# Optimization experiments

Hardware: AMD Instinct MI355X
Metric: run time of the kernel (lower is better)

## Reference

```python
import jax, jax.numpy as jnp
import numpy as np

# Dimensions
N = 100000      # nodes
E = 500000      # edges
D_IN = 128      # in_channels
H, C = 2, 64    # heads, out_channels per head (out_channels=128)
T = 128         # time_enc.out_channels
MSG = 128       # msg_dim
EDGE_DIM = MSG + T  # 256
SCALE = 1.0 / np.sqrt(C)


def setup_inputs() -> dict:
    key = jax.random.key(0)
    ks = jax.random.split(key, 16)
    s = 0.05
    x = jax.random.normal(ks[0], (N, D_IN), dtype=jnp.float32)
    last_update = jax.random.uniform(ks[1], (N,), dtype=jnp.float32)
    edge_index = jax.random.randint(ks[2], (2, E), 0, N, dtype=jnp.int64)
    t = jax.random.uniform(ks[3], (E,), dtype=jnp.float32) + 1.0  # event times >= last_update typically
    msg = jax.random.normal(ks[4], (E, MSG), dtype=jnp.float32)
    # TimeEncoder: cos(Linear(1, T))
    time_w = jax.random.normal(ks[5], (T, 1), dtype=jnp.float32) * s
    time_b = jax.random.normal(ks[6], (T,), dtype=jnp.float32) * s
    # TransformerConv linear layers (PyG defaults: q/k/v with bias, edge without, skip with bias)
    Wq = jax.random.normal(ks[7], (D_IN, H * C), dtype=jnp.float32) * s
    bq = jnp.zeros((H * C,), dtype=jnp.float32)
    Wk = jax.random.normal(ks[8], (D_IN, H * C), dtype=jnp.float32) * s
    bk = jnp.zeros((H * C,), dtype=jnp.float32)
    Wv = jax.random.normal(ks[9], (D_IN, H * C), dtype=jnp.float32) * s
    bv = jnp.zeros((H * C,), dtype=jnp.float32)
    We = jax.random.normal(ks[10], (EDGE_DIM, H * C), dtype=jnp.float32) * s
    Wskip = jax.random.normal(ks[11], (D_IN, H * C), dtype=jnp.float32) * s
    bskip = jnp.zeros((H * C,), dtype=jnp.float32)
    return dict(x=x, last_update=last_update, edge_index=edge_index, t=t, msg=msg,
                time_w=time_w, time_b=time_b, Wq=Wq, bq=bq, Wk=Wk, bk=bk,
                Wv=Wv, bv=bv, We=We, Wskip=Wskip, bskip=bskip)


def reference(x, last_update, edge_index, t, msg, time_w, time_b,
              Wq, bq, Wk, bk, Wv, bv, We, Wskip, bskip):
    src, dst = edge_index[0], edge_index[1]
    # relative time encoding: cos(Linear(1, T)(rel_t))
    rel_t = t - last_update[src]                                   # [E]
    rel_t_enc = jnp.cos(rel_t[:, None] * time_w[:, 0][None, :] + time_b)  # [E, T]
    edge_attr = jnp.concatenate([rel_t_enc, msg], axis=-1)         # [E, EDGE_DIM]

    # TransformerConv (heads=H, per-head dim C, eval mode so no dropout)
    q = (x @ Wq + bq).reshape(N, H, C)
    k = (x @ Wk + bk).reshape(N, H, C)
    v = (x @ Wv + bv).reshape(N, H, C)
    e = (edge_attr @ We).reshape(E, H, C)

    k_j = k[src] + e                                               # [E, H, C]
    logits = jnp.sum(q[dst] * k_j, axis=-1) * SCALE                # [E, H]

    # segment softmax over destination nodes
    m = jax.ops.segment_max(logits, dst, num_segments=N)           # [N, H]
    p = jnp.exp(logits - m[dst])
    denom = jax.ops.segment_sum(p, dst, num_segments=N)
    alpha = p / (denom[dst] + 1e-16)                               # [E, H]

    msgs = (v[src] + e) * alpha[..., None]                         # [E, H, C]
    out = jax.ops.segment_sum(msgs, dst, num_segments=N).reshape(N, H * C)
    # root/skip connection
    return out + x @ Wskip + bskip
```

## Files before the change

### kernel.cpp

```cpp
#include <hip/hip_runtime.h>
#include <math.h>


#define SCALE_ATTN 0.125f
#define SCAN_CHUNK 512

typedef __attribute__((ext_vector_type(8))) short bf16x8;
typedef __attribute__((ext_vector_type(4))) float f32x4;

union AFrag { bf16x8 v; unsigned short u[8]; };

__device__ __forceinline__ unsigned short f2bf(float f) {
    unsigned int u = __float_as_uint(f);
    u += 0x7fffu + ((u >> 16) & 1u);
    return (unsigned short)(u >> 16);
}
__device__ __forceinline__ float bf2f(unsigned int lo16) {
    return __uint_as_float(lo16 << 16);
}
__device__ __forceinline__ void unpack8(uint4 u, float* f) {
    f[0] = bf2f(u.x & 0xffffu); f[1] = bf2f(u.x >> 16);
    f[2] = bf2f(u.y & 0xffffu); f[3] = bf2f(u.y >> 16);
    f[4] = bf2f(u.z & 0xffffu); f[5] = bf2f(u.z >> 16);
    f[6] = bf2f(u.w & 0xffffu); f[7] = bf2f(u.w >> 16);
}
__device__ __forceinline__ bf16x8 pack2(float4 a, float4 b) {
    AFrag f;
    f.u[0] = f2bf(a.x); f.u[1] = f2bf(a.y); f.u[2] = f2bf(a.z); f.u[3] = f2bf(a.w);
    f.u[4] = f2bf(b.x); f.u[5] = f2bf(b.y); f.u[6] = f2bf(b.z); f.u[7] = f2bf(b.w);
    return f.v;
}

__global__ __launch_bounds__(256) void k_zero(int4* __restrict__ p, int n4)
{
    const int i = blockIdx.x * 256 + threadIdx.x;
    if (i < n4) p[i] = make_int4(0, 0, 0, 0);
}

__global__ __launch_bounds__(512, 4) void k_node_mfma(
    const float4* __restrict__ x4,
    const float* __restrict__ Wq, const float* __restrict__ Wk,
    const float* __restrict__ Wv, const float* __restrict__ Ws,
    const float* __restrict__ bq, const float* __restrict__ bk,
    const float* __restrict__ bv, const float* __restrict__ bs,
    unsigned short* __restrict__ qb, unsigned short* __restrict__ kb,
    unsigned short* __restrict__ vb, float* __restrict__ outp,
    int N, int numTiles)
{
    __shared__ __align__(16) unsigned short sX[32 * 128];
    const int tid = threadIdx.x;
    const int w = tid >> 6, l = tid & 63;
    const int l15 = l & 15, lg = l >> 4;
    const int mat = w >> 1;
    const int colbase = (w & 1) * 64;

    const float* Wm = (mat == 0) ? Wq : (mat == 1) ? Wk : (mat == 2) ? Wv : Ws;
    const float* bm = (mat == 0) ? bq : (mat == 1) ? bk : (mat == 2) ? bv : bs;

    bf16x8 Bf[4][4];
    float bias[4];
    #pragma unroll
    for (int nt = 0; nt < 4; ++nt) {
        const int col = colbase + nt * 16 + l15;
        bias[nt] = bm[col];
        #pragma unroll
        for (int ks = 0; ks < 4; ++ks) {
            AFrag f;
            #pragma unroll
            for (int j = 0; j < 8; ++j)
                f.u[j] = f2bf(Wm[(ks * 32 + lg * 8 + j) * 128 + col]);
            Bf[ks][nt] = f.v;
        }
    }

    for (int tile = blockIdx.x; tile < numTiles; tile += gridDim.x) {
        {
            const int e = tid >> 4, k8 = tid & 15;
            const int row = min(tile * 32 + e, N - 1);
            const float4 a0 = x4[(size_t)row * 32 + k8 * 2];
            const float4 a1 = x4[(size_t)row * 32 + k8 * 2 + 1];
            const int byteoff = (e * 256 + k8 * 16) ^ ((e & 7) << 4);
            *(bf16x8*)((char*)sX + byteoff) = pack2(a0, a1);
        }
        __syncthreads();

        f32x4 acc[2][4];
        #pragma unroll
        for (int m = 0; m < 2; ++m)
            #pragma unroll
            for (int nt = 0; nt < 4; ++nt) acc[m][nt] = (f32x4)(0.f);

        #pragma unroll
        for (int m = 0; m < 2; ++m) {
            const int lrow = m * 16 + l15;
            #pragma unroll
            for (int ks = 0; ks < 4; ++ks) {
                const int byteoff = (lrow * 256 + ks * 64 + lg * 16) ^ ((lrow & 7) << 4);
                const bf16x8 a = *(const bf16x8*)((const char*)sX + byteoff);
                #pragma unroll
                for (int nt = 0; nt < 4; ++nt)
                    acc[m][nt] = __builtin_amdgcn_mfma_f32_16x16x32_bf16(a, Bf[ks][nt], acc[m][nt], 0, 0, 0);
            }
        }

        #pragma unroll
        for (int m = 0; m < 2; ++m) {
            #pragma unroll
            for (int nt = 0; nt < 4; ++nt) {
                const int col = colbase + nt * 16 + l15;
                #pragma unroll
                for (int r = 0; r < 4; ++r) {
                    const int node = tile * 32 + m * 16 + lg * 4 + r;
                    if (node < N) {
                        const float val = acc[m][nt][r] + bias[nt];
                        if (mat == 0)      qb[(size_t)node * 128 + col] = f2bf(val);
                        else if (mat == 1) kb[(size_t)node * 128 + col] = f2bf(val);
                        else if (mat == 2) vb[(size_t)node * 128 + col] = f2bf(val);
                        else               outp[(size_t)node * 128 + col] = val;
                    }
                }
            }
        }
        __syncthreads();
    }
}

__global__ __launch_bounds__(512, 4) void k_edge_mfma(
    const float4* __restrict__ msg4,
    const float* __restrict__ relo,
    const float4* __restrict__ tw4, const float4* __restrict__ tb4,
    const float* __restrict__ We,
    unsigned short* __restrict__ ebuf, int E, int numTiles)
{
    __shared__ __align__(16) unsigned short sWe[128 * 256];
    __shared__ __align__(16) unsigned short sMsg[64 * 128];
    const int tid = threadIdx.x;
    const int w = tid >> 6, l = tid & 63;
    const int l15 = l & 15, lg = l >> 4;
    const int msub = w >> 1;
    const int colbase = (w & 1) * 64;

    for (int c = tid; c < 4096; c += 512) {
        const int n = c >> 5, k0 = (c & 31) << 3;
        AFrag af;
        #pragma unroll
        for (int j = 0; j < 8; ++j) af.u[j] = f2bf(We[(k0 + j) * 128 + n]);
        const int byteoff = ((n << 9) + (k0 << 1)) ^ ((n & 7) << 4);
        *(bf16x8*)((char*)sWe + byteoff) = af.v;
    }
    __syncthreads();

    const int nrow = colbase + l15;
    const int swzW = (nrow & 7) << 4;

    for (int tile = blockIdx.x; tile < numTiles; tile += gridDim.x) {
        const int ebase = tile * 64;

        #pragma unroll
        for (int i = 0; i < 2; ++i) {
            const int U = tid * 2 + i;
            const int e = U >> 4, u = U & 15;
            const int er = min(ebase + e, E - 1);
            const float4 a0 = msg4[(size_t)er * 32 + u * 2];
            const float4 a1 = msg4[(size_t)er * 32 + u * 2 + 1];
            const int byteoff = (e << 8) + ((u ^ (e & 7)) << 4);
            *(bf16x8*)((char*)sMsg + byteoff) = pack2(a0, a1);
        }
        __syncthreads();

        const int erow = ebase + msub * 16 + l15;
        const float rel = relo[min(erow, E - 1)];

        f32x4 acc[4];
        #pragma unroll
        for (int i = 0; i < 4; ++i) acc[i] = (f32x4)(0.f);

        #pragma unroll
        for (int kk = 0; kk < 4; ++kk) {
            const int kbase = (kk << 5) + (lg << 3);

            const float4 tww = tw4[kbase >> 2];
            const float4 tw2 = tw4[(kbase >> 2) + 1];
            const float4 tbb = tb4[kbase >> 2];
            const float4 tb2 = tb4[(kbase >> 2) + 1];
            AFrag a;
            a.u[0] = f2bf(__cosf(fmaf(rel, tww.x, tbb.x)));
            a.u[1] = f2bf(__cosf(fmaf(rel, tww.y, tbb.y)));
            a.u[2] = f2bf(__cosf(fmaf(rel, tww.z, tbb.z)));
            a.u[3] = f2bf(__cosf(fmaf(rel, tww.w, tbb.w)));
            a.u[4] = f2bf(__cosf(fmaf(rel, tw2.x, tb2.x)));
            a.u[5] = f2bf(__cosf(fmaf(rel, tw2.y, tb2.y)));
            a.u[6] = f2bf(__cosf(fmaf(rel, tw2.z, tb2.z)));
            a.u[7] = f2bf(__cosf(fmaf(rel, tw2.w, tb2.w)));
            const int bC = ((nrow << 9) + (kbase << 1)) ^ swzW;
            #pragma unroll
            for (int nt = 0; nt < 4; ++nt) {
                const bf16x8 b = *(const bf16x8*)((const char*)sWe + (bC + (nt << 13)));
                acc[nt] = __builtin_amdgcn_mfma_f32_16x16x32_bf16(a.v, b, acc[nt], 0, 0, 0);
            }

            const int me = msub * 16 + l15;
            const int mu = (kk << 2) + lg;
            const int mbyte = (me << 8) + ((mu ^ (me & 7)) << 4);
            const bf16x8 am = *(const bf16x8*)((const char*)sMsg + mbyte);
            const int bM = ((nrow << 9) + ((128 + kbase) << 1)) ^ swzW;
            #pragma unroll
            for (int nt = 0; nt < 4; ++nt) {
                const bf16x8 b = *(const bf16x8*)((const char*)sWe + (bM + (nt << 13)));
                acc[nt] = __builtin_amdgcn_mfma_f32_16x16x32_bf16(am, b, acc[nt], 0, 0, 0);
            }
        }

        #pragma unroll
        for (int nt = 0; nt < 4; ++nt) {
            const int col = colbase + nt * 16 + l15;
            #pragma unroll
            for (int r = 0; r < 4; ++r) {
                const int er = ebase + msub * 16 + (lg << 2) + r;
                if (er < E) ebuf[(size_t)er * 128 + col] = f2bf(acc[nt][r]);
            }
        }
        __syncthreads();
    }
}

__global__ __launch_bounds__(256) void k_hist(
    const int* __restrict__ ei, int* __restrict__ counts, int E)
{
    int i = blockIdx.x * 256 + threadIdx.x;
    if (i < E) atomicAdd(&counts[ei[E + i]], 1);
}

__global__ __launch_bounds__(256) void k_scan_partial(
    const int* __restrict__ counts, int* __restrict__ partial, int N)
{
    const int base = blockIdx.x * SCAN_CHUNK;
    int v = 0;
    for (int i = threadIdx.x; i < SCAN_CHUNK; i += 256) {
        const int idx = base + i;
        if (idx < N) v += counts[idx];
    }
    __shared__ int red[4];
    #pragma unroll
    for (int off = 1; off < 64; off <<= 1) v += __shfl_xor(v, off);
    if ((threadIdx.x & 63) == 0) red[threadIdx.x >> 6] = v;
    __syncthreads();
    if (threadIdx.x == 0) partial[blockIdx.x] = red[0] + red[1] + red[2] + red[3];
}

__global__ __launch_bounds__(256) void k_scan_base(
    const int* __restrict__ partial, int* __restrict__ base, int nb)
{
    __shared__ int tmp[256];
    const int v = (threadIdx.x < nb) ? partial[threadIdx.x] : 0;
    tmp[threadIdx.x] = v;
    __syncthreads();
    for (int off = 1; off < 256; off <<= 1) {
        const int add = (threadIdx.x >= off) ? tmp[threadIdx.x - off] : 0;
        __syncthreads();
        tmp[threadIdx.x] += add;
        __syncthreads();
    }
    if (threadIdx.x < nb) base[threadIdx.x] = tmp[threadIdx.x] - v;
}

__global__ __launch_bounds__(256) void k_scan_final(
    const int* __restrict__ counts, const int* __restrict__ base,
    int* __restrict__ rowptr, int* __restrict__ cursor, int N)
{
    const int i0 = blockIdx.x * SCAN_CHUNK;
    __shared__ int tmp[256];
    const int ia = i0 + threadIdx.x * 2, ib = ia + 1;
    const int v0 = (ia < N) ? counts[ia] : 0;
    const int v1 = (ib < N) ? counts[ib] : 0;
    const int s = v0 + v1;
    tmp[threadIdx.x] = s;
    __syncthreads();
    for (int off = 1; off < 256; off <<= 1) {
        const int add = (threadIdx.x >= off) ? tmp[threadIdx.x - off] : 0;
        __syncthreads();
        tmp[threadIdx.x] += add;
        __syncthreads();
    }
    const int excl = tmp[threadIdx.x] - s + base[blockIdx.x];
    if (ia < N) { rowptr[ia] = excl;      cursor[ia] = excl; }
    if (ib < N) { rowptr[ib] = excl + v0; cursor[ib] = excl + v0; }
}

__global__ __launch_bounds__(256) void k_fill(
    const int* __restrict__ ei, const float* __restrict__ t,
    const float* __restrict__ lu, int* __restrict__ cursor,
    int* __restrict__ perm, int* __restrict__ srcp,
    float* __restrict__ relo, int E)
{
    int i = blockIdx.x * 256 + threadIdx.x;
    if (i < E) {
        const int s = ei[i];
        const int d = ei[E + i];
        const int pos = atomicAdd(&cursor[d], 1);
        perm[pos] = i;
        srcp[pos] = s;
        relo[i] = t[i] - lu[s];
    }
}

__global__ __launch_bounds__(256) void k_agg(
    const int* __restrict__ srcp, const int* __restrict__ perm,
    const int* __restrict__ rowptr, const int* __restrict__ counts,
    const uint4* __restrict__ qb4, const uint4* __restrict__ kb4,
    const uint4* __restrict__ vb4, const uint4* __restrict__ eb4,
    float4* __restrict__ out4, int N)
{
    const int d = blockIdx.x * 4 + (threadIdx.x >> 6);
    if (d >= N) return;
    const int l = threadIdx.x & 63;
    const int s16 = l & 15;
    const int eg = l >> 4;
    const int start = rowptr[d];
    const int deg = counts[d];

    float qf[8];
    unpack8(qb4[(size_t)d * 16 + s16], qf);
    float accf[8] = {0.f, 0.f, 0.f, 0.f, 0.f, 0.f, 0.f, 0.f};
    float denom = 0.f;

    for (int cbase = 0; cbase < deg; cbase += 64) {
        const int clen = min(deg - cbase, 64);
        int mySrc = 0, myEid = 0;
        if (l < clen) {
            mySrc = srcp[start + cbase + l];
            myEid = perm[start + cbase + l];
        }

        #pragma unroll 2
        for (int i = 0; i < clen; i += 4) {
            const int off = i + eg;
            const bool valid = off < clen;
            const int offc = valid ? off : 0;
            const int src = __shfl(mySrc, offc);
            const int eid = __shfl(myEid, offc);
            float kf[8], ef[8], vf[8];
            unpack8(kb4[(size_t)src * 16 + s16], kf);
            unpack8(eb4[(size_t)eid * 16 + s16], ef);
            unpack8(vb4[(size_t)src * 16 + s16], vf);
            float s = 0.f;
            #pragma unroll
            for (int j = 0; j < 8; ++j) s = fmaf(qf[j], kf[j] + ef[j], s);
            s += __shfl_xor(s, 1);
            s += __shfl_xor(s, 2);
            s += __shfl_xor(s, 4);
            const float p = valid ? __expf(s * SCALE_ATTN) : 0.f;
            denom += p;
            #pragma unroll
            for (int j = 0; j < 8; ++j) accf[j] = fmaf(p, vf[j] + ef[j], accf[j]);
        }
    }
    #pragma unroll
    for (int j = 0; j < 8; ++j) {
        accf[j] += __shfl_xor(accf[j], 16);
        accf[j] += __shfl_xor(accf[j], 32);
    }
    denom += __shfl_xor(denom, 16);
    denom += __shfl_xor(denom, 32);

    if (l < 16) {
        const float inv = 1.f / (denom + 1e-16f);
        float4* o = out4 + (size_t)d * 32 + s16 * 2;
        const float4 c0 = o[0];
        const float4 c1 = o[1];
        o[0] = make_float4(fmaf(accf[0], inv, c0.x), fmaf(accf[1], inv, c0.y),
                           fmaf(accf[2], inv, c0.z), fmaf(accf[3], inv, c0.w));
        o[1] = make_float4(fmaf(accf[4], inv, c1.x), fmaf(accf[5], inv, c1.y),
                           fmaf(accf[6], inv, c1.z), fmaf(accf[7], inv, c1.w));
    }
}

extern "C" void kernel_launch(void* const* d_in, const int* in_sizes, int n_in,
                              void* d_out, int out_size, void* d_ws, size_t ws_size,
                              hipStream_t stream)
{
    const float* x   = (const float*)d_in[0];
    const float* lu  = (const float*)d_in[1];
    const int*   ei  = (const int*)d_in[2];
    const float* t   = (const float*)d_in[3];
    const float* msg = (const float*)d_in[4];
    const float* tw  = (const float*)d_in[5];
    const float* tb  = (const float*)d_in[6];
    const float* Wq  = (const float*)d_in[7];
    const float* bq  = (const float*)d_in[8];
    const float* Wk  = (const float*)d_in[9];
    const float* bk  = (const float*)d_in[10];
    const float* Wv  = (const float*)d_in[11];
    const float* bv  = (const float*)d_in[12];
    const float* We  = (const float*)d_in[13];
    const float* Wsk = (const float*)d_in[14];
    const float* bsk = (const float*)d_in[15];

    const int N = in_sizes[1];
    const int E = in_sizes[3];
    float* out = (float*)d_out;

    char* ws = (char*)d_ws;
    unsigned short* qb = (unsigned short*)ws;  ws += (size_t)N * 128 * sizeof(unsigned short);
    unsigned short* kb = (unsigned short*)ws;  ws += (size_t)N * 128 * sizeof(unsigned short);
    unsigned short* vb = (unsigned short*)ws;  ws += (size_t)N * 128 * sizeof(unsigned short);
    unsigned short* eb = (unsigned short*)ws;  ws += (size_t)E * 128 * sizeof(unsigned short);
    int*   counts  = (int*)ws;   ws += (size_t)N * sizeof(int);
    int*   rowptr  = (int*)ws;   ws += (size_t)N * sizeof(int);
    int*   cursor  = (int*)ws;   ws += (size_t)N * sizeof(int);
    int*   perm    = (int*)ws;   ws += (size_t)E * sizeof(int);
    int*   srcp    = (int*)ws;   ws += (size_t)E * sizeof(int);
    float* relo    = (float*)ws; ws += (size_t)E * sizeof(float);
    int*   partial = (int*)ws;   ws += 512 * sizeof(int);
    int*   baseArr = (int*)ws;   ws += 512 * sizeof(int);

    const int nScan = (N + SCAN_CHUNK - 1) / SCAN_CHUNK;

    const int n4 = (N + 3) / 4;
    k_zero<<<(n4 + 255) / 256, 256, 0, stream>>>((int4*)counts, n4);

    k_hist<<<(E + 255) / 256, 256, 0, stream>>>(ei, counts, E);
    k_scan_partial<<<nScan, 256, 0, stream>>>(counts, partial, N);
    k_scan_base<<<1, 256, 0, stream>>>(partial, baseArr, nScan);
    k_scan_final<<<nScan, 256, 0, stream>>>(counts, baseArr, rowptr, cursor, N);
    k_fill<<<(E + 255) / 256, 256, 0, stream>>>(ei, t, lu, cursor, perm, srcp, relo, E);

    const int nTN = (N + 31) / 32;
    k_node_mfma<<<min(nTN, 1024), 512, 0, stream>>>(
        (const float4*)x, Wq, Wk, Wv, Wsk, bq, bk, bv, bsk,
        qb, kb, vb, out, N, nTN);

    const int nTE = (E + 63) / 64;
    k_edge_mfma<<<min(nTE, 512), 512, 0, stream>>>(
        (const float4*)msg, relo,
        (const float4*)tw, (const float4*)tb, We, eb, E, nTE);

    k_agg<<<(N + 3) / 4, 256, 0, stream>>>(
        srcp, perm, rowptr, counts,
        (const uint4*)qb, (const uint4*)kb, (const uint4*)vb, (const uint4*)eb,
        (float4*)out, N);
}
```

Before: 368.1 us.

## Store skip projection as bf16, restructure edge GEMM waves, skip invalid edge loads

The node kernel now writes the skip projection to a bf16 workspace buffer instead of fp32 into the output, and the aggregation kernel reads that buffer rather than re-reading the fp32 output. The edge GEMM drops to 256 threads per block, with each wave handling two 16-row edge tiles so every LDS weight fragment feeds two MFMAs, halving weight LDS reads. The aggregation loop skips the gather loads for invalid lanes. The skip connection loses precision through bf16 rounding, and the edge kernel has fewer waves per block, which reduces latency hiding.

```diff
diff --git a/kernel.cpp b/kernel.cpp
--- a/kernel.cpp
+++ b/kernel.cpp
@@ -44,7 +44,7 @@
     const float* __restrict__ bq, const float* __restrict__ bk,
     const float* __restrict__ bv, const float* __restrict__ bs,
     unsigned short* __restrict__ qb, unsigned short* __restrict__ kb,
-    unsigned short* __restrict__ vb, float* __restrict__ outp,
+    unsigned short* __restrict__ vb, unsigned short* __restrict__ skb,
     int N, int numTiles)
 {
     __shared__ __align__(16) unsigned short sX[32 * 128];
@@ -56,6 +56,7 @@
 
     const float* Wm = (mat == 0) ? Wq : (mat == 1) ? Wk : (mat == 2) ? Wv : Ws;
     const float* bm = (mat == 0) ? bq : (mat == 1) ? bk : (mat == 2) ? bv : bs;
+    unsigned short* dst = (mat == 0) ? qb : (mat == 1) ? kb : (mat == 2) ? vb : skb;
 
     bf16x8 Bf[4][4];
     float bias[4];
@@ -111,13 +112,8 @@
                 #pragma unroll
                 for (int r = 0; r < 4; ++r) {
                     const int node = tile * 32 + m * 16 + lg * 4 + r;
-                    if (node < N) {
-                        const float val = acc[m][nt][r] + bias[nt];
-                        if (mat == 0)      qb[(size_t)node * 128 + col] = f2bf(val);
-                        else if (mat == 1) kb[(size_t)node * 128 + col] = f2bf(val);
-                        else if (mat == 2) vb[(size_t)node * 128 + col] = f2bf(val);
-                        else               outp[(size_t)node * 128 + col] = val;
-                    }
+                    if (node < N)
+                        dst[(size_t)node * 128 + col] = f2bf(acc[m][nt][r] + bias[nt]);
                 }
             }
         }
@@ -125,7 +121,7 @@
     }
 }
 
-__global__ __launch_bounds__(512, 4) void k_edge_mfma(
+__global__ __launch_bounds__(256, 2) void k_edge_mfma(
     const float4* __restrict__ msg4,
     const float* __restrict__ relo,
     const float4* __restrict__ tw4, const float4* __restrict__ tb4,
@@ -137,10 +133,10 @@
     const int tid = threadIdx.x;
     const int w = tid >> 6, l = tid & 63;
     const int l15 = l & 15, lg = l >> 4;
-    const int msub = w >> 1;
-    const int colbase = (w & 1) * 64;
-
-    for (int c = tid; c < 4096; c += 512) {
+    const int ch = w & 1;
+    const int mp = w >> 1;
+
+    for (int c = tid; c < 4096; c += 256) {
         const int n = c >> 5, k0 = (c & 31) << 3;
         AFrag af;
         #pragma unroll
@@ -150,15 +146,12 @@
     }
     __syncthreads();
 
-    const int nrow = colbase + l15;
-    const int swzW = (nrow & 7) << 4;
-
     for (int tile = blockIdx.x; tile < numTiles; tile += gridDim.x) {
         const int ebase = tile * 64;
 
         #pragma unroll
-        for (int i = 0; i < 2; ++i) {
-            const int U = tid * 2 + i;
+        for (int i = 0; i < 4; ++i) {
+            const int U = tid + i * 256;
             const int e = U >> 4, u = U & 15;
             const int er = min(ebase + e, E - 1);
             const float4 a0 = msg4[(size_t)er * 32 + u * 2];
@@ -168,12 +161,14 @@
         }
         __syncthreads();
 
-        const int erow = ebase + msub * 16 + l15;
-        const float rel = relo[min(erow, E - 1)];
-
-        f32x4 acc[4];
-        #pragma unroll
-        for (int i = 0; i < 4; ++i) acc[i] = (f32x4)(0.f);
+        const int r0 = mp * 32 + l15;
+        const int r1 = r0 + 16;
+        const float rel0 = relo[min(ebase + r0, E - 1)];
+        const float rel1 = relo[min(ebase + r1, E - 1)];
+
+        f32x4 acc0[4], acc1[4];
+        #pragma unroll
+        for (int i = 0; i < 4; ++i) { acc0[i] = (f32x4)(0.f); acc1[i] = (f32x4)(0.f); }
 
         #pragma unroll
         for (int kk = 0; kk < 4; ++kk) {
@@ -183,41 +178,54 @@
             const float4 tw2 = tw4[(kbase >> 2) + 1];
             const float4 tbb = tb4[kbase >> 2];
             const float4 tb2 = tb4[(kbase >> 2) + 1];
-            AFrag a;
-            a.u[0] = f2bf(__cosf(fmaf(rel, tww.x, tbb.x)));
-            a.u[1] = f2bf(__cosf(fmaf(rel, tww.y, tbb.y)));
-            a.u[2] = f2bf(__cosf(fmaf(rel, tww.z, tbb.z)));
-            a.u[3] = f2bf(__cosf(fmaf(rel, tww.w, tbb.w)));
-            a.u[4] = f2bf(__cosf(fmaf(rel, tw2.x, tb2.x)));
-            a.u[5] = f2bf(__cosf(fmaf(rel, tw2.y, tb2.y)));
-            a.u[6] = f2bf(__cosf(fmaf(rel, tw2.z, tb2.z)));
-            a.u[7] = f2bf(__cosf(fmaf(rel, tw2.w, tb2.w)));
-            const int bC = ((nrow << 9) + (kbase << 1)) ^ swzW;
+            AFrag a0, a1;
+            a0.u[0] = f2bf(__cosf(fmaf(rel0, tww.x, tbb.x)));
+            a0.u[1] = f2bf(__cosf(fmaf(rel0, tww.y, tbb.y)));
+            a0.u[2] = f2bf(__cosf(fmaf(rel0, tww.z, tbb.z)));
+            a0.u[3] = f2bf(__cosf(fmaf(rel0, tww.w, tbb.w)));
+            a0.u[4] = f2bf(__cosf(fmaf(rel0, tw2.x, tb2.x)));
+            a0.u[5] = f2bf(__cosf(fmaf(rel0, tw2.y, tb2.y)));
+            a0.u[6] = f2bf(__cosf(fmaf(rel0, tw2.z, tb2.z)));
+            a0.u[7] = f2bf(__cosf(fmaf(rel0, tw2.w, tb2.w)));
+            a1.u[0] = f2bf(__cosf(fmaf(rel1, tww.x, tbb.x)));
+            a1.u[1] = f2bf(__cosf(fmaf(rel1, tww.y, tbb.y)));
+            a1.u[2] = f2bf(__cosf(fmaf(rel1, tww.z, tbb.z)));
+            a1.u[3] = f2bf(__cosf(fmaf(rel1, tww.w, tbb.w)));
+            a1.u[4] = f2bf(__cosf(fmaf(rel1, tw2.x, tb2.x)));
+            a1.u[5] = f2bf(__cosf(fmaf(rel1, tw2.y, tb2.y)));
+            a1.u[6] = f2bf(__cosf(fmaf(rel1, tw2.z, tb2.z)));
+            a1.u[7] = f2bf(__cosf(fmaf(rel1, tw2.w, tb2.w)));
+
+            const int mu = (kk << 2) + lg;
+            const bf16x8 am0 = *(const bf16x8*)((const char*)sMsg +
+                                 ((r0 << 8) + ((mu ^ (r0 & 7)) << 4)));
+            const bf16x8 am1 = *(const bf16x8*)((const char*)sMsg +
+                                 ((r1 << 8) + ((mu ^ (r1 & 7)) << 4)));
+
             #pragma unroll
             for (int nt = 0; nt < 4; ++nt) {
-                const bf16x8 b = *(const bf16x8*)((const char*)sWe + (bC + (nt << 13)));
-                acc[nt] = __builtin_amdgcn_mfma_f32_16x16x32_bf16(a.v, b, acc[nt], 0, 0, 0);
+                const int nrow = ch * 64 + nt * 16 + l15;
+                const int swz = (nrow & 7) << 4;
+                const bf16x8 bC = *(const bf16x8*)((const char*)sWe +
+                                   (((nrow << 9) + (kbase << 1)) ^ swz));
+                acc0[nt] = __builtin_amdgcn_mfma_f32_16x16x32_bf16(a0.v, bC, acc0[nt], 0, 0, 0);
+                acc1[nt] = __builtin_amdgcn_mfma_f32_16x16x32_bf16(a1.v, bC, acc1[nt], 0, 0, 0);
+                const bf16x8 bM = *(const bf16x8*)((const char*)sWe +
+                                   (((nrow << 9) + ((128 + kbase) << 1)) ^ swz));
+                acc0[nt] = __builtin_amdgcn_mfma_f32_16x16x32_bf16(am0, bM, acc0[nt], 0, 0, 0);
+                acc1[nt] = __builtin_amdgcn_mfma_f32_16x16x32_bf16(am1, bM, acc1[nt], 0, 0, 0);
             }
-
-            const int me = msub * 16 + l15;
-            const int mu = (kk << 2) + lg;
-            const int mbyte = (me << 8) + ((mu ^ (me & 7)) << 4);
-            const bf16x8 am = *(const bf16x8*)((const char*)sMsg + mbyte);
-            const int bM = ((nrow << 9) + ((128 + kbase) << 1)) ^ swzW;
-            #pragma unroll
-            for (int nt = 0; nt < 4; ++nt) {
-                const bf16x8 b = *(const bf16x8*)((const char*)sWe + (bM + (nt << 13)));
-                acc[nt] = __builtin_amdgcn_mfma_f32_16x16x32_bf16(am, b, acc[nt], 0, 0, 0);
-            }
         }
 
         #pragma unroll
         for (int nt = 0; nt < 4; ++nt) {
-            const int col = colbase + nt * 16 + l15;
+            const int col = ch * 64 + nt * 16 + l15;
             #pragma unroll
             for (int r = 0; r < 4; ++r) {
-                const int er = ebase + msub * 16 + (lg << 2) + r;
-                if (er < E) ebuf[(size_t)er * 128 + col] = f2bf(acc[nt][r]);
+                const int e0 = ebase + mp * 32 + (lg << 2) + r;
+                const int e1 = e0 + 16;
+                if (e0 < E) ebuf[(size_t)e0 * 128 + col] = f2bf(acc0[nt][r]);
+                if (e1 < E) ebuf[(size_t)e1 * 128 + col] = f2bf(acc1[nt][r]);
             }
         }
         __syncthreads();
@@ -309,7 +317,7 @@
     const int* __restrict__ rowptr, const int* __restrict__ counts,
     const uint4* __restrict__ qb4, const uint4* __restrict__ kb4,
     const uint4* __restrict__ vb4, const uint4* __restrict__ eb4,
-    float4* __restrict__ out4, int N)
+    const uint4* __restrict__ skb4, float4* __restrict__ out4, int N)
 {
     const int d = blockIdx.x * 4 + (threadIdx.x >> 6);
     if (d >= N) return;
@@ -339,20 +347,22 @@
             const int offc = valid ? off : 0;
             const int src = __shfl(mySrc, offc);
             const int eid = __shfl(myEid, offc);
-            float kf[8], ef[8], vf[8];
-            unpack8(kb4[(size_t)src * 16 + s16], kf);
-            unpack8(eb4[(size_t)eid * 16 + s16], ef);
-            unpack8(vb4[(size_t)src * 16 + s16], vf);
-            float s = 0.f;
-            #pragma unroll
-            for (int j = 0; j < 8; ++j) s = fmaf(qf[j], kf[j] + ef[j], s);
-            s += __shfl_xor(s, 1);
-            s += __shfl_xor(s, 2);
-            s += __shfl_xor(s, 4);
-            const float p = valid ? __expf(s * SCALE_ATTN) : 0.f;
-            denom += p;
-            #pragma unroll
-            for (int j = 0; j < 8; ++j) accf[j] = fmaf(p, vf[j] + ef[j], accf[j]);
+            if (valid) {
+                float kf[8], ef[8], vf[8];
+                unpack8(kb4[(size_t)src * 16 + s16], kf);
+                unpack8(eb4[(size_t)eid * 16 + s16], ef);
+                unpack8(vb4[(size_t)src * 16 + s16], vf);
+                float s = 0.f;
+                #pragma unroll
+                for (int j = 0; j < 8; ++j) s = fmaf(qf[j], kf[j] + ef[j], s);
+                s += __shfl_xor(s, 1);
+                s += __shfl_xor(s, 2);
+                s += __shfl_xor(s, 4);
+                const float p = __expf(s * SCALE_ATTN);
+                denom += p;
+                #pragma unroll
+                for (int j = 0; j < 8; ++j) accf[j] = fmaf(p, vf[j] + ef[j], accf[j]);
+            }
         }
     }
     #pragma unroll
@@ -365,13 +375,13 @@
 
     if (l < 16) {
         const float inv = 1.f / (denom + 1e-16f);
+        float sk[8];
+        unpack8(skb4[(size_t)d * 16 + s16], sk);
         float4* o = out4 + (size_t)d * 32 + s16 * 2;
-        const float4 c0 = o[0];
-        const float4 c1 = o[1];
-        o[0] = make_float4(fmaf(accf[0], inv, c0.x), fmaf(accf[1], inv, c0.y),
-                           fmaf(accf[2], inv, c0.z), fmaf(accf[3], inv, c0.w));
-        o[1] = make_float4(fmaf(accf[4], inv, c1.x), fmaf(accf[5], inv, c1.y),
-                           fmaf(accf[6], inv, c1.z), fmaf(accf[7], inv, c1.w));
+        o[0] = make_float4(fmaf(accf[0], inv, sk[0]), fmaf(accf[1], inv, sk[1]),
+                           fmaf(accf[2], inv, sk[2]), fmaf(accf[3], inv, sk[3]));
+        o[1] = make_float4(fmaf(accf[4], inv, sk[4]), fmaf(accf[5], inv, sk[5]),
+                           fmaf(accf[6], inv, sk[6]), fmaf(accf[7], inv, sk[7]));
     }
 }
 
@@ -401,10 +411,11 @@
     float* out = (float*)d_out;
 
     char* ws = (char*)d_ws;
-    unsigned short* qb = (unsigned short*)ws;  ws += (size_t)N * 128 * sizeof(unsigned short);
-    unsigned short* kb = (unsigned short*)ws;  ws += (size_t)N * 128 * sizeof(unsigned short);
-    unsigned short* vb = (unsigned short*)ws;  ws += (size_t)N * 128 * sizeof(unsigned short);
-    unsigned short* eb = (unsigned short*)ws;  ws += (size_t)E * 128 * sizeof(unsigned short);
+    unsigned short* qb  = (unsigned short*)ws;  ws += (size_t)N * 128 * sizeof(unsigned short);
+    unsigned short* kb  = (unsigned short*)ws;  ws += (size_t)N * 128 * sizeof(unsigned short);
+    unsigned short* vb  = (unsigned short*)ws;  ws += (size_t)N * 128 * sizeof(unsigned short);
+    unsigned short* skb = (unsigned short*)ws;  ws += (size_t)N * 128 * sizeof(unsigned short);
+    unsigned short* eb  = (unsigned short*)ws;  ws += (size_t)E * 128 * sizeof(unsigned short);
     int*   counts  = (int*)ws;   ws += (size_t)N * sizeof(int);
     int*   rowptr  = (int*)ws;   ws += (size_t)N * sizeof(int);
     int*   cursor  = (int*)ws;   ws += (size_t)N * sizeof(int);
@@ -428,15 +439,15 @@
     const int nTN = (N + 31) / 32;
     k_node_mfma<<<min(nTN, 1024), 512, 0, stream>>>(
         (const float4*)x, Wq, Wk, Wv, Wsk, bq, bk, bv, bsk,
-        qb, kb, vb, out, N, nTN);
+        qb, kb, vb, skb, N, nTN);
 
     const int nTE = (E + 63) / 64;
-    k_edge_mfma<<<min(nTE, 512), 512, 0, stream>>>(
+    k_edge_mfma<<<min(nTE, 512), 256, 0, stream>>>(
         (const float4*)msg, relo,
         (const float4*)tw, (const float4*)tb, We, eb, E, nTE);
 
     k_agg<<<(N + 3) / 4, 256, 0, stream>>>(
         srcp, perm, rowptr, counts,
         (const uint4*)qb, (const uint4*)kb, (const uint4*)vb, (const uint4*)eb,
-        (float4*)out, N);
-}
+        (const uint4*)skb, (float4*)out, N);
+}
```

Result: faster. 342.2 us (-7.0%).
